# Performance work log

Hardware: AMD Instinct MI355X
Metric: run time of the kernel (lower is better)

The kernel has to match this reference:

```python
import jax, jax.numpy as jnp
import numpy as np

N_USERS = 100000
N_ITEMS = 50000
N_NODES = N_USERS + N_ITEMS
N_EDGES = 4800000
EMB_DIM = 64
N_LAYERS = 3


def setup_inputs() -> dict:
    key = jax.random.key(0)
    k1, k2, k3, k4, k5 = jax.random.split(key, 5)
    adj_rows = jax.random.randint(k1, (N_EDGES,), 0, N_NODES, dtype=jnp.int64 if jax.config.jax_enable_x64 else jnp.int32)
    adj_cols = jax.random.randint(k2, (N_EDGES,), 0, N_NODES, dtype=jnp.int64 if jax.config.jax_enable_x64 else jnp.int32)
    adj_vals = jax.random.uniform(k3, (N_EDGES,), dtype=jnp.float32)
    user_emb = jax.random.normal(k4, (N_USERS, EMB_DIM), dtype=jnp.float32)
    item_emb = jax.random.normal(k5, (N_ITEMS, EMB_DIM), dtype=jnp.float32)
    return {"adj_rows": adj_rows, "adj_cols": adj_cols, "adj_vals": adj_vals,
            "user_emb": user_emb, "item_emb": item_emb}


def _spmm(rows, cols, vals, x):
    # sparse.mm(adj, x): gather source node features, scale by edge value,
    # scatter-add into destination rows. Shapes: [E] indices, [N, D] features.
    msgs = vals[:, None] * x[cols]          # [E, D]
    return jax.ops.segment_sum(msgs, rows, num_segments=N_NODES)  # [N, D]


def reference(adj_rows, adj_cols, adj_vals, user_emb, item_emb):
    all_emb = jnp.concatenate([user_emb, item_emb], axis=0)  # [N, D]
    acc = all_emb                                            # running sum over layers (fused stack+mean)
    emb = all_emb
    for _ in range(N_LAYERS):
        emb = _spmm(adj_rows, adj_cols, adj_vals, emb)
        acc = acc + emb
    final = acc / jnp.asarray(N_LAYERS + 1, dtype=acc.dtype)
    return final[:N_USERS], final[N_USERS:]
```

## Files before the change

kernel.cpp:

```cpp
#include <hip/hip_runtime.h>


#define N_USERS 100000
#define N_ITEMS 50000
#define N_NODES 150000
#define N_EDGES 4800000
#define EMB_DIM 64

typedef unsigned short u16;
typedef unsigned int   u32;

constexpr int NODE_FLOATS  = N_NODES * EMB_DIM;
constexpr int NODE_FLOAT4S = NODE_FLOATS / 4;
constexpr int USER_FLOAT4S = N_USERS * EMB_DIM / 4;

constexpr int BSH  = 7;
constexpr int BRW  = 128;
constexpr int NB   = (N_NODES + BRW - 1) / BRW;
constexpr int NXG  = 8;
constexpr int SEG  = NB * NXG;
constexpr int CAP1 = 704;
constexpr int EPB  = 6144;
constexpr int ABLK2 = (N_EDGES + EPB - 1) / EPB;
constexpr int SB_CAP2 = 5760;
constexpr int CSR_CAP = 6000000;

static __device__ __forceinline__ float bf2f(u16 b) {
    return __uint_as_float(((u32)b) << 16);
}
static __device__ __forceinline__ u16 f2bf(float f) {
    u32 u = __float_as_uint(f);
    return (u16)((u + 0x7FFFu + ((u >> 16) & 1u)) >> 16);
}

__global__ void prelude_kernel(const float* __restrict__ user_emb,
                               const float* __restrict__ item_emb,
                               u16* __restrict__ emb,
                               int* __restrict__ bx_pos,
                               int* __restrict__ csr_cursor) {
    int i = blockIdx.x * blockDim.x + threadIdx.x;
    if (i < SEG) bx_pos[i * 16] = i * CAP1;
    if (i == 0) csr_cursor[0] = 0;
    if (i >= NODE_FLOAT4S) return;
    float4 v = (i < USER_FLOAT4S) ? ((const float4*)user_emb)[i]
                                  : ((const float4*)item_emb)[i - USER_FLOAT4S];
    ushort4 o;
    o.x = f2bf(v.x); o.y = f2bf(v.y); o.z = f2bf(v.z); o.w = f2bf(v.w);
    ((ushort4*)emb)[i] = o;
}

__global__ void stageA2_kernel(const int* __restrict__ rows,
                               const int* __restrict__ cols,
                               const float* __restrict__ vals,
                               int* __restrict__ bx_pos,
                               u32* __restrict__ stage_key,
                               u16* __restrict__ stage_val) {
    __shared__ u32 lkey[EPB];
    __shared__ u16 lval[EPB];
    __shared__ u16 lbkt[EPB];
    __shared__ int hist[NB];
    __shared__ int hstart[NB];
    __shared__ int hcur[NB];
    __shared__ int gbase[NB];
    __shared__ int ws4[4];

    const int tid  = threadIdx.x;
    const int base = blockIdx.x * EPB;
    const int cnt  = min(EPB, N_EDGES - base);
    const int x    = blockIdx.x & (NXG - 1);

    for (int i = tid; i < NB; i += 256) hist[i] = 0;
    __syncthreads();

    for (int k = 0; k < EPB / 256; k += 8) {
        int rbuf[8];
        #pragma unroll
        for (int q = 0; q < 8; ++q) {
            int idx = (k + q) * 256 + tid;
            rbuf[q] = (idx < cnt) ? rows[base + idx] : -1;
        }
        #pragma unroll
        for (int q = 0; q < 8; ++q)
            if (rbuf[q] >= 0) atomicAdd(&hist[rbuf[q] >> BSH], 1);
    }
    __syncthreads();

    const int lane = tid & 63, wave = tid >> 6;
    int carry = 0;
    for (int c0 = 0; c0 < NB; c0 += 256) {
        int i = c0 + tid;
        int v = (i < NB) ? hist[i] : 0;
        int incl = v;
        #pragma unroll
        for (int off = 1; off < 64; off <<= 1) {
            int t = __shfl_up(incl, off);
            if (lane >= off) incl += t;
        }
        if (lane == 63) ws4[wave] = incl;
        __syncthreads();
        int wpref = 0, tot = 0;
        #pragma unroll
        for (int w = 0; w < 4; ++w) { int s = ws4[w]; if (w < wave) wpref += s; tot += s; }
        int excl = carry + wpref + incl - v;
        if (i < NB) { hstart[i] = excl; hcur[i] = excl; }
        carry += tot;
        __syncthreads();
    }

    for (int k = 0; k < EPB / 256; k += 8) {
        int rb[8], cb[8]; float vb[8];
        #pragma unroll
        for (int q = 0; q < 8; ++q) {
            int idx = (k + q) * 256 + tid;
            if (idx < cnt) { rb[q] = rows[base + idx]; cb[q] = cols[base + idx]; vb[q] = vals[base + idx]; }
            else rb[q] = -1;
        }
        #pragma unroll
        for (int q = 0; q < 8; ++q) {
            if (rb[q] < 0) continue;
            int b = rb[q] >> BSH;
            int p = atomicAdd(&hcur[b], 1);
            lkey[p] = ((u32)(rb[q] & (BRW - 1)) << 24) | (u32)cb[q];
            lval[p] = f2bf(vb[q]);
            lbkt[p] = (u16)b;
        }
    }
    __syncthreads();

    for (int i = tid; i < NB; i += 256) {
        int n = hist[i];
        if (n) {
            int seg = i * NXG + x;
            int p = atomicAdd(&bx_pos[seg * 16], n);
            gbase[i] = (p + n <= (seg + 1) * CAP1) ? p : -1;
        }
    }
    __syncthreads();

    for (int i = tid; i < cnt; i += 256) {
        int b  = lbkt[i];
        int gb = gbase[b];
        if (gb >= 0) {
            int d = gb + (i - hstart[b]);
            stage_key[d] = lkey[i];
            stage_val[d] = lval[i];
        }
    }
}

__global__ void stageB2_kernel(const int* __restrict__ bx_pos,
                               const u32* __restrict__ stage_key,
                               const u16* __restrict__ stage_val,
                               int* __restrict__ csr_cursor,
                               u32* __restrict__ csr_col,
                               u16* __restrict__ csr_val,
                               u32* __restrict__ desc) {
    __shared__ u32 skey[SB_CAP2];
    __shared__ u16 sval[SB_CAP2];
    __shared__ int rhist[256], rpad0[256], rcur[256];
    __shared__ int ws4[4];
    __shared__ int sbase_sh;

    const int b   = blockIdx.x;
    const int tid = threadIdx.x;
    rhist[tid] = 0;
    __syncthreads();

    for (int xx = 0; xx < NXG; ++xx) {
        int seg = b * NXG + xx;
        int sb  = seg * CAP1;
        int n   = min(bx_pos[seg * 16] - sb, CAP1);
        for (int i = tid; i < n; i += 256)
            atomicAdd(&rhist[stage_key[sb + i] >> 24], 1);
    }
    __syncthreads();

    const int lane = tid & 63, wave = tid >> 6;
    int v  = rhist[tid];
    int vp = (v + 15) & ~15;
    int incl = vp;
    #pragma unroll
    for (int off = 1; off < 64; off <<= 1) {
        int t = __shfl_up(incl, off);
        if (lane >= off) incl += t;
    }
    if (lane == 63) ws4[wave] = incl;
    __syncthreads();
    int wpref = 0, total = 0;
    #pragma unroll
    for (int w = 0; w < 4; ++w) { int s = ws4[w]; if (w < wave) wpref += s; total += s; }
    int excl = wpref + incl - vp;
    rpad0[tid] = excl;
    rcur[tid]  = excl;
    if (tid == 0) sbase_sh = atomicAdd(csr_cursor, total);
    __syncthreads();

    const int tcap = min(total, SB_CAP2);
    for (int i = tid; i < tcap; i += 256) { skey[i] = 0u; sval[i] = 0; }
    __syncthreads();

    for (int xx = 0; xx < NXG; ++xx) {
        int seg = b * NXG + xx;
        int sb  = seg * CAP1;
        int n   = min(bx_pos[seg * 16] - sb, CAP1);
        for (int i = tid; i < n; i += 256) {
            u32 key = stage_key[sb + i];
            u16 val = stage_val[sb + i];
            int p = atomicAdd(&rcur[key >> 24], 1);
            if (p < SB_CAP2) { skey[p] = key & 0x00FFFFFFu; sval[p] = val; }
        }
    }
    __syncthreads();

    const int sbase = sbase_sh;
    for (int i = tid; i < tcap; i += 256) {
        int g = sbase + i;
        if (g < CSR_CAP) { csr_col[g] = skey[i]; csr_val[g] = sval[i]; }
    }
    if (tid < BRW) {
        int grow = b * BRW + tid;
        if (grow < N_NODES) {
            int cp = vp; if (cp > 240) cp = 240;
            desc[grow] = ((u32)(sbase + rpad0[tid]) << 8) | (u32)cp;
        }
    }
}

__global__ __launch_bounds__(256, 8)
void spmm_rw_kernel(const u32* __restrict__ desc,
                    const u32* __restrict__ csr_col,
                    const u16* __restrict__ csr_val,
                    const u16* __restrict__ x,
                    u16* __restrict__ y,
                    const u16* __restrict__ e0,
                    const u16* __restrict__ y1,
                    const u16* __restrict__ y2,
                    float* __restrict__ out) {
    const int lane = threadIdx.x & 63;
    const int wid  = __builtin_amdgcn_readfirstlane(threadIdx.x >> 6);
    const int row  = blockIdx.x * 4 + wid;
    if (row >= N_NODES) return;

    const u32 d   = desc[row];
    const int beg = (int)(d >> 8);
    const int nch = (int)(d & 255u) >> 4;

    const u32* __restrict__ pc = csr_col + beg;
    const u32* __restrict__ pv = ((const u32*)csr_val) + (beg >> 1);
    const u16* __restrict__ xl = x + lane;

    float a[4] = {0.f, 0.f, 0.f, 0.f};

    for (int ch = 0; ch < nch; ++ch) {
        u32 c[16];
        u32 w[8];
        #pragma unroll
        for (int k = 0; k < 16; ++k) c[k] = pc[ch * 16 + k];
        #pragma unroll
        for (int k = 0; k < 8; ++k)  w[k] = pv[ch * 8 + k];

        u32 xv[16];
        #pragma unroll
        for (int k = 0; k < 16; ++k)
            xv[k] = (u32)xl[(size_t)c[k] * EMB_DIM];

        #pragma unroll
        for (int k = 0; k < 16; ++k) {
            u32 vb = (k & 1) ? (w[k >> 1] & 0xFFFF0000u) : (w[k >> 1] << 16);
            float vv = __uint_as_float(vb);
            float xf = __uint_as_float(xv[k] << 16);
            a[k & 3] += vv * xf;
        }
    }
    float s = (a[0] + a[1]) + (a[2] + a[3]);

    size_t oidx = (size_t)row * EMB_DIM + lane;
    if (y) {
        y[oidx] = f2bf(s);
    } else {
        float r = (bf2f(e0[oidx]) + bf2f(y1[oidx]) + bf2f(y2[oidx]) + s) * 0.25f;
        out[oidx] = r;
    }
}

__global__ void init3_kernel(const float* __restrict__ user_emb,
                             const float* __restrict__ item_emb,
                             float* __restrict__ emb,
                             float* __restrict__ acc,
                             float* __restrict__ nxt) {
    int i = blockIdx.x * blockDim.x + threadIdx.x;
    if (i >= NODE_FLOAT4S) return;
    float4 v = (i < USER_FLOAT4S) ? ((const float4*)user_emb)[i]
                                  : ((const float4*)item_emb)[i - USER_FLOAT4S];
    ((float4*)emb)[i] = v;
    ((float4*)acc)[i] = v;
    ((float4*)nxt)[i] = make_float4(0.f, 0.f, 0.f, 0.f);
}

__global__ void spmm_atomic_kernel(const int* __restrict__ rows,
                                   const int* __restrict__ cols,
                                   const float* __restrict__ vals,
                                   const float* __restrict__ x,
                                   float* __restrict__ y) {
    unsigned tid = blockIdx.x * blockDim.x + threadIdx.x;
    unsigned e  = tid >> 4;
    unsigned d4 = tid & 15u;
    if (e >= N_EDGES) return;
    int r = rows[e]; int c = cols[e]; float v = vals[e];
    float4 xv = ((const float4*)(x + (size_t)c * EMB_DIM))[d4];
    float* yp = y + (size_t)r * EMB_DIM + d4 * 4;
    atomicAdd(yp + 0, v * xv.x);
    atomicAdd(yp + 1, v * xv.y);
    atomicAdd(yp + 2, v * xv.z);
    atomicAdd(yp + 3, v * xv.w);
}

__global__ void acc_kernel(float* __restrict__ acc, const float* __restrict__ nxt,
                           float* __restrict__ zbuf, int do_zero, float scale) {
    int i = blockIdx.x * blockDim.x + threadIdx.x;
    if (i >= NODE_FLOAT4S) return;
    float4 a = ((float4*)acc)[i];
    float4 n = ((const float4*)nxt)[i];
    a.x = (a.x + n.x) * scale; a.y = (a.y + n.y) * scale;
    a.z = (a.z + n.z) * scale; a.w = (a.w + n.w) * scale;
    ((float4*)acc)[i] = a;
    if (do_zero) ((float4*)zbuf)[i] = make_float4(0.f, 0.f, 0.f, 0.f);
}

extern "C" void kernel_launch(void* const* d_in, const int* in_sizes, int n_in,
                              void* d_out, int out_size, void* d_ws, size_t ws_size,
                              hipStream_t stream) {
    const int*   rows     = (const int*)d_in[0];
    const int*   cols     = (const int*)d_in[1];
    const float* vals     = (const float*)d_in[2];
    const float* user_emb = (const float*)d_in[3];
    const float* item_emb = (const float*)d_in[4];
    float* out = (float*)d_out;

    constexpr size_t U_BUF   = (size_t)NODE_FLOATS / 2;
    constexpr size_t U_SKEY  = (size_t)SEG * CAP1;
    constexpr size_t U_SVAL  = U_SKEY / 2;
    constexpr size_t U_STAGE = U_SKEY + U_SVAL;
    constexpr size_t U_CCOL  = (size_t)CSR_CAP;
    constexpr size_t U_CVAL  = (size_t)CSR_CAP / 2;
    size_t need_u32 = U_BUF + U_STAGE + U_CCOL + U_CVAL + (size_t)N_NODES
                    + (size_t)SEG * 16 + 16;

    const int EW_BLOCKS = (NODE_FLOAT4S + 255) / 256;

    if (ws_size >= need_u32 * 4) {
        u32* W = (u32*)d_ws;
        u16* buf0      = (u16*)W;
        u32* stage_key = W + U_BUF;
        u16* stage_val = (u16*)(W + U_BUF + U_SKEY);
        u16* buf1      = (u16*)(W + U_BUF);
        u16* buf2      = (u16*)(W + U_BUF + U_BUF);
        u32* csr_col   = W + U_BUF + U_STAGE;
        u16* csr_val   = (u16*)(csr_col + U_CCOL);
        u32* desc      = (u32*)(csr_col + U_CCOL + U_CVAL);
        int* bx_pos    = (int*)(desc + N_NODES);
        int* csr_cur   = bx_pos + (size_t)SEG * 16;

        prelude_kernel<<<EW_BLOCKS, 256, 0, stream>>>(user_emb, item_emb, buf0,
                                                      bx_pos, csr_cur);
        stageA2_kernel<<<ABLK2, 256, 0, stream>>>(rows, cols, vals, bx_pos,
                                                  stage_key, stage_val);
        stageB2_kernel<<<NB, 256, 0, stream>>>(bx_pos, stage_key, stage_val,
                                               csr_cur, csr_col, csr_val, desc);

        const int SPMM_BLOCKS = (N_NODES + 3) / 4;
        spmm_rw_kernel<<<SPMM_BLOCKS, 256, 0, stream>>>(desc, csr_col, csr_val,
                                                        buf0, buf1, nullptr, nullptr, nullptr, nullptr);
        spmm_rw_kernel<<<SPMM_BLOCKS, 256, 0, stream>>>(desc, csr_col, csr_val,
                                                        buf1, buf2, nullptr, nullptr, nullptr, nullptr);
        spmm_rw_kernel<<<SPMM_BLOCKS, 256, 0, stream>>>(desc, csr_col, csr_val,
                                                        buf2, nullptr, buf0, buf1, buf2, out);
    } else {
        float* buf0 = (float*)d_ws;
        float* buf1 = buf0 + NODE_FLOATS;
        const int SPMM_BLOCKS = (int)(((size_t)N_EDGES * 16 + 255) / 256);
        init3_kernel<<<EW_BLOCKS, 256, 0, stream>>>(user_emb, item_emb, buf0, out, buf1);
        float* prev = buf0; float* next = buf1;
        for (int layer = 0; layer < 3; ++layer) {
            spmm_atomic_kernel<<<SPMM_BLOCKS, 256, 0, stream>>>(rows, cols, vals, prev, next);
            if (layer < 2) acc_kernel<<<EW_BLOCKS, 256, 0, stream>>>(out, next, prev, 1, 1.0f);
            else           acc_kernel<<<EW_BLOCKS, 256, 0, stream>>>(out, next, prev, 0, 0.25f);
            float* t = prev; prev = next; next = t;
        }
    }
}
```

Before: 490.7 us.

## Replace atomic segment staging with per-block bucketed runs and offset table

```diff
diff --git a/kernel.cpp b/kernel.cpp
--- a/kernel.cpp
+++ b/kernel.cpp
@@ -17,11 +17,9 @@
 constexpr int BSH  = 7;
 constexpr int BRW  = 128;
 constexpr int NB   = (N_NODES + BRW - 1) / BRW;
-constexpr int NXG  = 8;
-constexpr int SEG  = NB * NXG;
-constexpr int CAP1 = 704;
 constexpr int EPB  = 6144;
 constexpr int ABLK2 = (N_EDGES + EPB - 1) / EPB;
+constexpr int HSW  = NB + 1;
 constexpr int SB_CAP2 = 5760;
 constexpr int CSR_CAP = 6000000;
 
@@ -36,10 +34,8 @@
 __global__ void prelude_kernel(const float* __restrict__ user_emb,
                                const float* __restrict__ item_emb,
                                u16* __restrict__ emb,
-                               int* __restrict__ bx_pos,
                                int* __restrict__ csr_cursor) {
     int i = blockIdx.x * blockDim.x + threadIdx.x;
-    if (i < SEG) bx_pos[i * 16] = i * CAP1;
     if (i == 0) csr_cursor[0] = 0;
     if (i >= NODE_FLOAT4S) return;
     float4 v = (i < USER_FLOAT4S) ? ((const float4*)user_emb)[i]
@@ -52,22 +48,19 @@
 __global__ void stageA2_kernel(const int* __restrict__ rows,
                                const int* __restrict__ cols,
                                const float* __restrict__ vals,
-                               int* __restrict__ bx_pos,
-                               u32* __restrict__ stage_key,
-                               u16* __restrict__ stage_val) {
+                               uint2* __restrict__ stage_rec,
+                               u32* __restrict__ hs) {
     __shared__ u32 lkey[EPB];
     __shared__ u16 lval[EPB];
     __shared__ u16 lbkt[EPB];
     __shared__ int hist[NB];
     __shared__ int hstart[NB];
     __shared__ int hcur[NB];
-    __shared__ int gbase[NB];
     __shared__ int ws4[4];
 
     const int tid  = threadIdx.x;
     const int base = blockIdx.x * EPB;
     const int cnt  = min(EPB, N_EDGES - base);
-    const int x    = blockIdx.x & (NXG - 1);
 
     for (int i = tid; i < NB; i += 256) hist[i] = 0;
     __syncthreads();
@@ -126,31 +119,19 @@
         }
     }
     __syncthreads();
-
-    for (int i = tid; i < NB; i += 256) {
-        int n = hist[i];
-        if (n) {
-            int seg = i * NXG + x;
-            int p = atomicAdd(&bx_pos[seg * 16], n);
-            gbase[i] = (p + n <= (seg + 1) * CAP1) ? p : -1;
-        }
-    }
-    __syncthreads();
-
-    for (int i = tid; i < cnt; i += 256) {
-        int b  = lbkt[i];
-        int gb = gbase[b];
-        if (gb >= 0) {
-            int d = gb + (i - hstart[b]);
-            stage_key[d] = lkey[i];
-            stage_val[d] = lval[i];
-        }
-    }
-}
-
-__global__ void stageB2_kernel(const int* __restrict__ bx_pos,
-                               const u32* __restrict__ stage_key,
-                               const u16* __restrict__ stage_val,
+    (void)lbkt;
+
+    uint2* __restrict__ dst = stage_rec + (size_t)blockIdx.x * EPB;
+    for (int i = tid; i < cnt; i += 256)
+        dst[i] = make_uint2(lkey[i], (u32)lval[i]);
+
+    u32* __restrict__ hrow = hs + (size_t)blockIdx.x * HSW;
+    for (int i = tid; i < NB; i += 256) hrow[i] = (u32)hstart[i];
+    if (tid == 0) hrow[NB] = (u32)cnt;
+}
+
+__global__ void stageB2_kernel(const uint2* __restrict__ stage_rec,
+                               const u32* __restrict__ hs,
                                int* __restrict__ csr_cursor,
                                u32* __restrict__ csr_col,
                                u16* __restrict__ csr_val,
@@ -166,12 +147,12 @@
     rhist[tid] = 0;
     __syncthreads();
 
-    for (int xx = 0; xx < NXG; ++xx) {
-        int seg = b * NXG + xx;
-        int sb  = seg * CAP1;
-        int n   = min(bx_pos[seg * 16] - sb, CAP1);
-        for (int i = tid; i < n; i += 256)
-            atomicAdd(&rhist[stage_key[sb + i] >> 24], 1);
+    for (int a = tid; a < ABLK2; a += 256) {
+        const u32* hp = hs + (size_t)a * HSW + b;
+        u32 s = hp[0], e = hp[1];
+        const uint2* rp = stage_rec + (size_t)a * EPB;
+        for (u32 i = s; i < e; ++i)
+            atomicAdd(&rhist[rp[i].x >> 24], 1);
     }
     __syncthreads();
 
@@ -199,15 +180,14 @@
     for (int i = tid; i < tcap; i += 256) { skey[i] = 0u; sval[i] = 0; }
     __syncthreads();
 
-    for (int xx = 0; xx < NXG; ++xx) {
-        int seg = b * NXG + xx;
-        int sb  = seg * CAP1;
-        int n   = min(bx_pos[seg * 16] - sb, CAP1);
-        for (int i = tid; i < n; i += 256) {
-            u32 key = stage_key[sb + i];
-            u16 val = stage_val[sb + i];
-            int p = atomicAdd(&rcur[key >> 24], 1);
-            if (p < SB_CAP2) { skey[p] = key & 0x00FFFFFFu; sval[p] = val; }
+    for (int a = tid; a < ABLK2; a += 256) {
+        const u32* hp = hs + (size_t)a * HSW + b;
+        u32 s = hp[0], e = hp[1];
+        const uint2* rp = stage_rec + (size_t)a * EPB;
+        for (u32 i = s; i < e; ++i) {
+            uint2 r = rp[i];
+            int p = atomicAdd(&rcur[r.x >> 24], 1);
+            if (p < SB_CAP2) { skey[p] = r.x & 0x00FFFFFFu; sval[p] = (u16)r.y; }
         }
     }
     __syncthreads();
@@ -337,36 +317,31 @@
     const float* item_emb = (const float*)d_in[4];
     float* out = (float*)d_out;
 
-    constexpr size_t U_BUF   = (size_t)NODE_FLOATS / 2;
-    constexpr size_t U_SKEY  = (size_t)SEG * CAP1;
-    constexpr size_t U_SVAL  = U_SKEY / 2;
-    constexpr size_t U_STAGE = U_SKEY + U_SVAL;
-    constexpr size_t U_CCOL  = (size_t)CSR_CAP;
-    constexpr size_t U_CVAL  = (size_t)CSR_CAP / 2;
-    size_t need_u32 = U_BUF + U_STAGE + U_CCOL + U_CVAL + (size_t)N_NODES
-                    + (size_t)SEG * 16 + 16;
+    constexpr size_t U_BUF  = (size_t)NODE_FLOATS / 2;
+    constexpr size_t U_SREC = (size_t)ABLK2 * EPB * 2;
+    constexpr size_t U_HS   = (size_t)ABLK2 * HSW;
+    constexpr size_t U_CCOL = (size_t)CSR_CAP;
+    constexpr size_t U_CVAL = (size_t)CSR_CAP / 2;
+    size_t need_u32 = U_BUF + U_SREC + U_HS + U_CCOL + U_CVAL + (size_t)N_NODES + 16;
 
     const int EW_BLOCKS = (NODE_FLOAT4S + 255) / 256;
 
     if (ws_size >= need_u32 * 4) {
         u32* W = (u32*)d_ws;
-        u16* buf0      = (u16*)W;
-        u32* stage_key = W + U_BUF;
-        u16* stage_val = (u16*)(W + U_BUF + U_SKEY);
-        u16* buf1      = (u16*)(W + U_BUF);
-        u16* buf2      = (u16*)(W + U_BUF + U_BUF);
-        u32* csr_col   = W + U_BUF + U_STAGE;
-        u16* csr_val   = (u16*)(csr_col + U_CCOL);
-        u32* desc      = (u32*)(csr_col + U_CCOL + U_CVAL);
-        int* bx_pos    = (int*)(desc + N_NODES);
-        int* csr_cur   = bx_pos + (size_t)SEG * 16;
-
-        prelude_kernel<<<EW_BLOCKS, 256, 0, stream>>>(user_emb, item_emb, buf0,
-                                                      bx_pos, csr_cur);
-        stageA2_kernel<<<ABLK2, 256, 0, stream>>>(rows, cols, vals, bx_pos,
-                                                  stage_key, stage_val);
-        stageB2_kernel<<<NB, 256, 0, stream>>>(bx_pos, stage_key, stage_val,
-                                               csr_cur, csr_col, csr_val, desc);
+        u16*   buf0      = (u16*)W;
+        uint2* stage_rec = (uint2*)(W + U_BUF);
+        u16*   buf1      = (u16*)(W + U_BUF);
+        u16*   buf2      = (u16*)(W + U_BUF + U_BUF);
+        u32*   hs        = W + U_BUF + U_SREC;
+        u32*   csr_col   = hs + U_HS;
+        u16*   csr_val   = (u16*)(csr_col + U_CCOL);
+        u32*   desc      = (u32*)(csr_col + U_CCOL + U_CVAL);
+        int*   csr_cur   = (int*)(desc + N_NODES);
+
+        prelude_kernel<<<EW_BLOCKS, 256, 0, stream>>>(user_emb, item_emb, buf0, csr_cur);
+        stageA2_kernel<<<ABLK2, 256, 0, stream>>>(rows, cols, vals, stage_rec, hs);
+        stageB2_kernel<<<NB, 256, 0, stream>>>(stage_rec, hs, csr_cur,
+                                               csr_col, csr_val, desc);
 
         const int SPMM_BLOCKS = (N_NODES + 3) / 4;
         spmm_rw_kernel<<<SPMM_BLOCKS, 256, 0, stream>>>(desc, csr_col, csr_val,
```

Measured after the change: 522.1 us. 1.06x slower.

## Fuse embedding bf16 conversion into edge staging kernel and memset counters

Applied to the files above, without the earlier changes.

```diff
diff --git a/kernel.cpp b/kernel.cpp
--- a/kernel.cpp
+++ b/kernel.cpp
@@ -20,8 +20,9 @@
 constexpr int NXG  = 8;
 constexpr int SEG  = NB * NXG;
 constexpr int CAP1 = 704;
-constexpr int EPB  = 6144;
+constexpr int EPB  = 4096;
 constexpr int ABLK2 = (N_EDGES + EPB - 1) / EPB;
+constexpr int CONV4 = 2048;
 constexpr int SB_CAP2 = 5760;
 constexpr int CSR_CAP = 6000000;
 
@@ -33,25 +34,12 @@
     return (u16)((u + 0x7FFFu + ((u >> 16) & 1u)) >> 16);
 }
 
-__global__ void prelude_kernel(const float* __restrict__ user_emb,
-                               const float* __restrict__ item_emb,
-                               u16* __restrict__ emb,
-                               int* __restrict__ bx_pos,
-                               int* __restrict__ csr_cursor) {
-    int i = blockIdx.x * blockDim.x + threadIdx.x;
-    if (i < SEG) bx_pos[i * 16] = i * CAP1;
-    if (i == 0) csr_cursor[0] = 0;
-    if (i >= NODE_FLOAT4S) return;
-    float4 v = (i < USER_FLOAT4S) ? ((const float4*)user_emb)[i]
-                                  : ((const float4*)item_emb)[i - USER_FLOAT4S];
-    ushort4 o;
-    o.x = f2bf(v.x); o.y = f2bf(v.y); o.z = f2bf(v.z); o.w = f2bf(v.w);
-    ((ushort4*)emb)[i] = o;
-}
-
 __global__ void stageA2_kernel(const int* __restrict__ rows,
                                const int* __restrict__ cols,
                                const float* __restrict__ vals,
+                               const float* __restrict__ user_emb,
+                               const float* __restrict__ item_emb,
+                               u16* __restrict__ emb,
                                int* __restrict__ bx_pos,
                                u32* __restrict__ stage_key,
                                u16* __restrict__ stage_val) {
@@ -69,6 +57,22 @@
     const int cnt  = min(EPB, N_EDGES - base);
     const int x    = blockIdx.x & (NXG - 1);
 
+    {
+        const int cbase = blockIdx.x * CONV4;
+        #pragma unroll
+        for (int q = 0; q < CONV4 / 256; ++q) {
+            int i = cbase + q * 256 + tid;
+            if (i < NODE_FLOAT4S) {
+                float4 v = (i < USER_FLOAT4S)
+                    ? ((const float4*)user_emb)[i]
+                    : ((const float4*)item_emb)[i - USER_FLOAT4S];
+                ushort4 o;
+                o.x = f2bf(v.x); o.y = f2bf(v.y); o.z = f2bf(v.z); o.w = f2bf(v.w);
+                ((ushort4*)emb)[i] = o;
+            }
+        }
+    }
+
     for (int i = tid; i < NB; i += 256) hist[i] = 0;
     __syncthreads();
 
@@ -132,7 +136,7 @@
         if (n) {
             int seg = i * NXG + x;
             int p = atomicAdd(&bx_pos[seg * 16], n);
-            gbase[i] = (p + n <= (seg + 1) * CAP1) ? p : -1;
+            gbase[i] = (p + n <= CAP1) ? (seg * CAP1 + p) : -1;
         }
     }
     __syncthreads();
@@ -169,7 +173,7 @@
     for (int xx = 0; xx < NXG; ++xx) {
         int seg = b * NXG + xx;
         int sb  = seg * CAP1;
-        int n   = min(bx_pos[seg * 16] - sb, CAP1);
+        int n   = min(bx_pos[seg * 16], CAP1);
         for (int i = tid; i < n; i += 256)
             atomicAdd(&rhist[stage_key[sb + i] >> 24], 1);
     }
@@ -202,7 +206,7 @@
     for (int xx = 0; xx < NXG; ++xx) {
         int seg = b * NXG + xx;
         int sb  = seg * CAP1;
-        int n   = min(bx_pos[seg * 16] - sb, CAP1);
+        int n   = min(bx_pos[seg * 16], CAP1);
         for (int i = tid; i < n; i += 256) {
             u32 key = stage_key[sb + i];
             u16 val = stage_val[sb + i];
@@ -359,12 +363,12 @@
         u16* csr_val   = (u16*)(csr_col + U_CCOL);
         u32* desc      = (u32*)(csr_col + U_CCOL + U_CVAL);
         int* bx_pos    = (int*)(desc + N_NODES);
-        int* csr_cur   = bx_pos + (size_t)SEG * 16;
-
-        prelude_kernel<<<EW_BLOCKS, 256, 0, stream>>>(user_emb, item_emb, buf0,
-                                                      bx_pos, csr_cur);
-        stageA2_kernel<<<ABLK2, 256, 0, stream>>>(rows, cols, vals, bx_pos,
-                                                  stage_key, stage_val);
+
+        hipMemsetAsync(bx_pos, 0, ((size_t)SEG * 16 + 16) * sizeof(int), stream);
+        stageA2_kernel<<<ABLK2, 256, 0, stream>>>(rows, cols, vals,
+                                                  user_emb, item_emb, buf0,
+                                                  bx_pos, stage_key, stage_val);
+        int* csr_cur = bx_pos + (size_t)SEG * 16;
         stageB2_kernel<<<NB, 256, 0, stream>>>(bx_pos, stage_key, stage_val,
                                                csr_cur, csr_col, csr_val, desc);
 
```

After: 502.5 us. 1.02x slower.
